# Kernel tuning notes

Hardware: AMD Instinct MI355X
Metric: run time of the kernel (lower is better)

The kernel has to match this reference:

```python
import jax, jax.numpy as jnp
from jax import lax
import numpy as np
import math

DIM = 96      # channels
HEADS = 3     # num_heads
WS = 8        # window size
SHIFT = 4     # window_size // 2 (depth is odd -> shifted)
TLC = 64      # tlc_kernel
H = 264
W = 264


def _grid_idxes(h, w, k1, k2):
    # Faithful replication of the torch grids() tiling index logic (static ints).
    num_row = (h - 1) // k1 + 1
    num_col = (w - 1) // k2 + 1
    step_j = k2 if num_col == 1 else math.ceil((w - k2) / (num_col - 1) - 1e-8)
    step_i = k1 if num_row == 1 else math.ceil((h - k1) / (num_row - 1) - 1e-8)
    idxes = []
    i = 0
    last_i = False
    while i < h and not last_i:
        j = 0
        if i + k1 >= h:
            i = h - k1
            last_i = True
        last_j = False
        while j < w and not last_j:
            if j + k2 >= w:
                j = w - k2
                last_j = True
            idxes.append((i, j))
            j = j + step_j
        i = i + step_i
    return idxes


def setup_inputs() -> dict:
    key = jax.random.key(0)
    ks = jax.random.split(key, 4)
    return {
        "x": jax.random.normal(ks[0], (1, DIM, H, W), jnp.float32),
        "temperature": jnp.ones((HEADS, 1, 1), jnp.float32),
        "qkv_w": jax.random.normal(ks[1], (3 * DIM, DIM), jnp.float32) * 0.05,
        "dw_w": jax.random.normal(ks[2], (3 * DIM, 1, 3, 3), jnp.float32) * 0.1,
        "proj_w": jax.random.normal(ks[3], (DIM, DIM), jnp.float32) * 0.05,
    }


def reference(x, temperature, qkv_w, dw_w, proj_w):
    b, c, h, w = x.shape
    # depth % 2 == 1 -> cyclic shift
    x = jnp.roll(x, (-SHIFT, -SHIFT), axis=(2, 3))
    # 1x1 pointwise conv (no bias)
    qkv = jnp.einsum('oc,bchw->bohw', qkv_w, x)
    # 3x3 depthwise conv, padding 1
    qkv = lax.conv_general_dilated(
        qkv, dw_w, window_strides=(1, 1), padding=[(1, 1), (1, 1)],
        feature_group_count=3 * c, dimension_numbers=('NCHW', 'OIHW', 'NCHW'))
    # --- TLC grids: overlapping tiles (eval path, b == 1) ---
    k1, k2 = min(h, TLC), min(w, TLC)
    idxes = _grid_idxes(h, w, k1, k2)
    parts = jnp.concatenate([qkv[:, :, i:i + k1, j:j + k2] for (i, j) in idxes], axis=0)  # [T,3c,k1,k2]
    T, C3, th, tw = parts.shape
    nh, nw = th // WS, tw // WS
    # window partition: b c (h b0) (w b1) -> (b h w) c b0 b1 -> flatten spatial
    win = parts.reshape(T, C3, nh, WS, nw, WS).transpose(0, 2, 4, 1, 3, 5)
    win = win.reshape(T * nh * nw, C3, WS * WS)  # [Bw, 3c, 64]
    q, k, v = jnp.split(win, 3, axis=1)  # each [Bw, c, 64]
    ch = c // HEADS
    q = q.reshape(-1, HEADS, ch, WS * WS)
    k = k.reshape(-1, HEADS, ch, WS * WS)
    v = v.reshape(-1, HEADS, ch, WS * WS)
    # L2 normalize along token dim (F.normalize eps=1e-12)
    q = q / jnp.maximum(jnp.linalg.norm(q, axis=-1, keepdims=True), 1e-12)
    k = k / jnp.maximum(jnp.linalg.norm(k, axis=-1, keepdims=True), 1e-12)
    # channel attention: [Bw, head, ch, ch]
    attn = jax.nn.relu(jnp.einsum('bhcn,bhdn->bhcd', q, k) * temperature)
    out = jnp.einsum('bhcd,bhdn->bhcn', attn, v)  # [Bw, head, ch, 64]
    out = out.reshape(-1, c, WS, WS)
    # window merge back to tiles
    out = out.reshape(T, nh, nw, c, WS, WS).transpose(0, 3, 1, 4, 2, 5).reshape(T, c, th, tw)
    # --- TLC grids_inverse: scatter-add overlapping tiles and average ---
    preds = jnp.zeros((b, c, h, w), x.dtype)
    cnt = np.zeros((h, w), np.float32)
    for t, (i, j) in enumerate(idxes):
        preds = preds.at[0, :, i:i + k1, j:j + k2].add(out[t])
        cnt[i:i + k1, j:j + k2] += 1.0
    preds = preds / jnp.asarray(cnt)
    # 1x1 output projection
    out = jnp.einsum('oc,bchw->bohw', proj_w, preds)
    # undo cyclic shift
    return jnp.roll(out, (SHIFT, SHIFT), axis=(2, 3))
```

## Files before the change

kernel.cpp:

```cpp
#include <hip/hip_runtime.h>
#include <hip/hip_bf16.h>

#define HW_ 69696
#define W_ 264
#define H_ 264

typedef short bf16x8 __attribute__((ext_vector_type(8)));
typedef float f32x4 __attribute__((ext_vector_type(4)));

static __device__ __forceinline__ unsigned short f2b(float f) {
  __hip_bfloat16 h = __float2bfloat16(f);
  return *reinterpret_cast<unsigned short*>(&h);
}
static __device__ __forceinline__ float b2f(unsigned short u) {
  __hip_bfloat16 h;
  *reinterpret_cast<unsigned short*>(&h) = u;
  return __bfloat162float(h);
}
static __device__ __forceinline__ float lo_f(unsigned int u) {
  union { unsigned int i; float f; } c; c.i = u << 16; return c.f;
}
static __device__ __forceinline__ float hi_f(unsigned int u) {
  union { unsigned int i; float f; } c; c.i = u & 0xffff0000u; return c.f;
}

__global__ __launch_bounds__(256, 3) void k_gemm(const float* __restrict__ x,
                                                 const float* __restrict__ w,
                                                 unsigned short* __restrict__ outb) {
  __shared__ __align__(16) char smem[46592];
  __shared__ int rp[128];
  unsigned short* As = (unsigned short*)smem;
  unsigned short* Bs = As + 96 * 104;

  const int tid = threadIdx.x;
  const int px0 = blockIdx.x * 128;
  const int oc = blockIdx.y;

  if (tid < 128) {
    int p = px0 + tid;
    int r = 0;
    if (p < HW_) {
      int y = p / W_, xx = p - y * W_;
      int y2 = y + 4; if (y2 >= H_) y2 -= H_;
      int x2 = xx + 4; if (x2 >= W_) x2 -= W_;
      r = y2 * W_ + x2;
    }
    rp[tid] = r;
  }

  const float* wp = w + oc * 96 * 96;
  for (int l = tid; l < 96 * 24; l += 256) {
    int o = l / 24, c4 = (l - (l / 24) * 24) * 4;
    float4 v = *(const float4*)&wp[o * 96 + c4];
    unsigned int p0 = (unsigned int)f2b(v.x) | ((unsigned int)f2b(v.y) << 16);
    unsigned int p1 = (unsigned int)f2b(v.z) | ((unsigned int)f2b(v.w) << 16);
    *(uint2*)&As[o * 104 + c4] = make_uint2(p0, p1);
  }
  __syncthreads();

  for (int l = tid; l < 128 * 12; l += 256) {
    int pxl = l & 127, g = l >> 7;
    uint4 o = make_uint4(0u, 0u, 0u, 0u);
    if (px0 + pxl < HW_) {
      const int base = rp[pxl];
      const float* xp = x + (size_t)(g * 8) * HW_ + base;
      float f0 = xp[0];
      float f1 = xp[HW_];
      float f2 = xp[2 * HW_];
      float f3 = xp[3 * HW_];
      float f4 = xp[4 * HW_];
      float f5 = xp[5 * HW_];
      float f6 = xp[6 * HW_];
      float f7 = xp[7 * HW_];
      o.x = (unsigned int)f2b(f0) | ((unsigned int)f2b(f1) << 16);
      o.y = (unsigned int)f2b(f2) | ((unsigned int)f2b(f3) << 16);
      o.z = (unsigned int)f2b(f4) | ((unsigned int)f2b(f5) << 16);
      o.w = (unsigned int)f2b(f6) | ((unsigned int)f2b(f7) << 16);
    }
    *(uint4*)&Bs[pxl * 104 + g * 8] = o;
  }
  __syncthreads();

  const int wid = tid >> 6, lane = tid & 63;
  const int quad = lane >> 4, lo = lane & 15;
  f32x4 acc[6][2];
#pragma unroll
  for (int mt = 0; mt < 6; ++mt)
#pragma unroll
    for (int nt = 0; nt < 2; ++nt) acc[mt][nt] = {0.f, 0.f, 0.f, 0.f};

#pragma unroll
  for (int ks = 0; ks < 3; ++ks) {
    const int kb = ks * 32 + quad * 8;
    bf16x8 b[2];
#pragma unroll
    for (int nt = 0; nt < 2; ++nt)
      b[nt] = *(const bf16x8*)&Bs[(wid * 32 + nt * 16 + lo) * 104 + kb];
#pragma unroll
    for (int mt = 0; mt < 6; ++mt) {
      bf16x8 a = *(const bf16x8*)&As[(mt * 16 + lo) * 104 + kb];
#pragma unroll
      for (int nt = 0; nt < 2; ++nt)
        acc[mt][nt] = __builtin_amdgcn_mfma_f32_16x16x32_bf16(a, b[nt], acc[mt][nt], 0, 0, 0);
    }
  }

  __syncthreads();
  unsigned short* Cs2 = (unsigned short*)smem;
#pragma unroll
  for (int mt = 0; mt < 6; ++mt)
#pragma unroll
    for (int nt = 0; nt < 2; ++nt) {
      int px_l = wid * 32 + nt * 16 + lo;
#pragma unroll
      for (int r = 0; r < 4; ++r)
        Cs2[px_l * 104 + mt * 16 + quad * 4 + r] = f2b(acc[mt][nt][r]);
    }
  __syncthreads();
  for (int i = tid; i < 128 * 12; i += 256) {
    int pxl = i & 127, j = i >> 7;
    if (px0 + pxl < HW_)
      *((uint4*)outb + (size_t)(oc * 12 + j) * HW_ + px0 + pxl) =
          ((const uint4*)(Cs2 + pxl * 104))[j];
  }
}

__global__ __launch_bounds__(256) void k_dw(const unsigned short* __restrict__ qkv,
                                            const float* __restrict__ dw,
                                            unsigned short* __restrict__ out) {
  __shared__ __align__(16) uint4 inS[18 * 66];
  const int tid = threadIdx.x;
  const int x0 = blockIdx.x * 64;
  const int y0 = blockIdx.y * 16;
  const int u = blockIdx.z;
  const uint4* plane = (const uint4*)qkv + (size_t)u * HW_;
  const float* wp = dw + u * 72;
  float wv[72];
#pragma unroll
  for (int i = 0; i < 72; ++i) wv[i] = wp[i];

  for (int idx = tid; idx < 18 * 66; idx += 256) {
    int rr = idx / 66, cc = idx - rr * 66;
    int gy = y0 - 1 + rr, gx = x0 - 1 + cc;
    uint4 v = make_uint4(0u, 0u, 0u, 0u);
    if ((unsigned)gy < (unsigned)H_ && (unsigned)gx < (unsigned)W_)
      v = plane[gy * W_ + gx];
    inS[idx] = v;
  }
  __syncthreads();

#pragma unroll
  for (int k = 0; k < 4; ++k) {
    const int oidx = k * 256 + tid;
    const int ro = oidx >> 6, co = oidx & 63;
    const int y = y0 + ro, x = x0 + co;
    float acc[8] = {0.f, 0.f, 0.f, 0.f, 0.f, 0.f, 0.f, 0.f};
#pragma unroll
    for (int dy = 0; dy < 3; ++dy)
#pragma unroll
      for (int dx = 0; dx < 3; ++dx) {
        uint4 v = inS[(ro + dy) * 66 + co + dx];
        float w0 = wv[0 * 9 + dy * 3 + dx], w1 = wv[1 * 9 + dy * 3 + dx];
        float w2 = wv[2 * 9 + dy * 3 + dx], w3 = wv[3 * 9 + dy * 3 + dx];
        float w4 = wv[4 * 9 + dy * 3 + dx], w5 = wv[5 * 9 + dy * 3 + dx];
        float w6 = wv[6 * 9 + dy * 3 + dx], w7 = wv[7 * 9 + dy * 3 + dx];
        acc[0] += w0 * lo_f(v.x); acc[1] += w1 * hi_f(v.x);
        acc[2] += w2 * lo_f(v.y); acc[3] += w3 * hi_f(v.y);
        acc[4] += w4 * lo_f(v.z); acc[5] += w5 * hi_f(v.z);
        acc[6] += w6 * lo_f(v.w); acc[7] += w7 * hi_f(v.w);
      }
    if (y < H_ && x < W_) {
      uint4 o;
      o.x = (unsigned int)f2b(acc[0]) | ((unsigned int)f2b(acc[1]) << 16);
      o.y = (unsigned int)f2b(acc[2]) | ((unsigned int)f2b(acc[3]) << 16);
      o.z = (unsigned int)f2b(acc[4]) | ((unsigned int)f2b(acc[5]) << 16);
      o.w = (unsigned int)f2b(acc[6]) | ((unsigned int)f2b(acc[7]) << 16);
      *((uint4*)out + (size_t)u * HW_ + y * W_ + x) = o;
    }
  }
}

#define P1 200
#define P8 1608
__global__ __launch_bounds__(192) void k_attn(const unsigned short* __restrict__ qd,
                                              const float* __restrict__ temp,
                                              unsigned short* __restrict__ tout) {
  __shared__ __align__(16) unsigned short flat[8 * P8];
  __shared__ __align__(16) unsigned short attnL[3 * 32 * 40];
  __shared__ float invn[3 * 32];
  const int tid = threadIdx.x;
  const int wi = blockIdx.x, t = blockIdx.y;
  const int i0 = (t / 5) * 50, j0 = (t % 5) * 50;
  const int wy = wi >> 3, wx = wi & 7;
  const int gy0 = i0 + wy * 8, gx0 = j0 + wx * 8;

  {
    const size_t base = (size_t)gy0 * W_ + gx0;
    for (int idx = tid; idx < 24 * 64; idx += 192) {
      int u = idx >> 6, rj = idx & 63, r = rj >> 3, j = rj & 7;
      uint4 v = ((const uint4*)qd)[(size_t)u * HW_ + base + r * W_ + j];
      ((uint4*)flat)[r * 201 + j * 25 + u] = v;
    }
  }
  __syncthreads();

  const int h = tid >> 6, lane = tid & 63;
  const int quad = lane >> 4, lo = lane & 15;
  const int cb = h * 32;

  bf16x8 qf[2][2], kf[2][2];
#pragma unroll
  for (int mt = 0; mt < 2; ++mt)
#pragma unroll
    for (int kt = 0; kt < 2; ++kt) {
      const int rbase = (kt * 4 + quad) * P8;
      const int cq = cb + mt * 16 + lo;
      const int ck = 96 + cb + mt * 16 + lo;
      bf16x8 q8, k8;
#pragma unroll
      for (int j = 0; j < 8; ++j) {
        q8[j] = (short)flat[rbase + j * P1 + cq];
        k8[j] = (short)flat[rbase + j * P1 + ck];
      }
      qf[mt][kt] = q8;
      kf[mt][kt] = k8;
    }

  f32x4 S[2][2];
#pragma unroll
  for (int mt = 0; mt < 2; ++mt)
#pragma unroll
    for (int nt = 0; nt < 2; ++nt) {
      S[mt][nt] = {0.f, 0.f, 0.f, 0.f};
#pragma unroll
      for (int kt = 0; kt < 2; ++kt)
        S[mt][nt] = __builtin_amdgcn_mfma_f32_16x16x32_bf16(qf[mt][kt], kf[nt][kt], S[mt][nt], 0, 0, 0);
    }

  float ivk[2];
#pragma unroll
  for (int mt = 0; mt < 2; ++mt) {
    float sq = 0.f, sk = 0.f;
#pragma unroll
    for (int kt = 0; kt < 2; ++kt)
#pragma unroll
      for (int j = 0; j < 8; ++j) {
        float a = b2f((unsigned short)qf[mt][kt][j]);
        float b = b2f((unsigned short)kf[mt][kt][j]);
        sq += a * a;
        sk += b * b;
      }
    sq += __shfl_xor(sq, 16);
    sq += __shfl_xor(sq, 32);
    sk += __shfl_xor(sk, 16);
    sk += __shfl_xor(sk, 32);
    if (quad == 0) invn[h * 32 + mt * 16 + lo] = 1.f / fmaxf(sqrtf(sq), 1e-12f);
    ivk[mt] = 1.f / fmaxf(sqrtf(sk), 1e-12f);
  }
  __syncthreads();

  const float ts = temp[h];
#pragma unroll
  for (int mt = 0; mt < 2; ++mt)
#pragma unroll
    for (int nt = 0; nt < 2; ++nt)
#pragma unroll
      for (int r = 0; r < 4; ++r) {
        int c = mt * 16 + quad * 4 + r;
        float v = S[mt][nt][r] * invn[h * 32 + c] * ivk[nt] * ts;
        attnL[(h * 32 + c) * 40 + nt * 16 + lo] = f2b(fmaxf(v, 0.f));
      }
  __syncthreads();

  bf16x8 af[2];
#pragma unroll
  for (int mt = 0; mt < 2; ++mt)
    af[mt] = *(const bf16x8*)&attnL[(h * 32 + mt * 16 + lo) * 40 + quad * 8];

  const int uv = 24 + h * 4 + quad;
  f32x4 O[2][4];
#pragma unroll
  for (int nt = 0; nt < 4; ++nt) {
    const int px = nt * 16 + lo;
    const size_t gpx = (size_t)(gy0 + (px >> 3)) * W_ + gx0 + (px & 7);
    uint4 vraw = ((const uint4*)qd)[(size_t)uv * HW_ + gpx];
    bf16x8 vf = *reinterpret_cast<bf16x8*>(&vraw);
#pragma unroll
    for (int mt = 0; mt < 2; ++mt) {
      f32x4 z = {0.f, 0.f, 0.f, 0.f};
      O[mt][nt] = __builtin_amdgcn_mfma_f32_16x16x32_bf16(af[mt], vf, z, 0, 0, 0);
    }
  }
  __syncthreads();

  unsigned short* Cs = flat;
#pragma unroll
  for (int mt = 0; mt < 2; ++mt)
#pragma unroll
    for (int nt = 0; nt < 4; ++nt) {
      const int px = nt * 16 + lo;
      unsigned int p0 = (unsigned int)f2b(O[mt][nt][0]) | ((unsigned int)f2b(O[mt][nt][1]) << 16);
      unsigned int p1 = (unsigned int)f2b(O[mt][nt][2]) | ((unsigned int)f2b(O[mt][nt][3]) << 16);
      *(uint2*)&Cs[px * 104 + cb + mt * 16 + quad * 4] = make_uint2(p0, p1);
    }
  __syncthreads();

  for (int idx = tid; idx < 64 * 12; idx += 192) {
    int rec = idx / 12, u = idx - (idx / 12) * 12;
    int r = rec >> 3, j = rec & 7;
    size_t g = (size_t)t * 4096 + (wy * 8 + r) * 64 + wx * 8 + j;
    ((uint4*)tout)[g * 12 + u] = ((const uint4*)(Cs + rec * 104))[u];
  }
}

__global__ __launch_bounds__(256, 4) void k_avgproj(const float* __restrict__ w,
                                                    const unsigned short* __restrict__ tout,
                                                    float* __restrict__ outf) {
  __shared__ __align__(16) char smem[33280];
  unsigned short* As = (unsigned short*)smem;
  unsigned short* Bs = As + 96 * 104;

  const int tid = threadIdx.x;
  const int px0 = blockIdx.x * 64;

  for (int l = tid; l < 96 * 24; l += 256) {
    int o = l / 24, c4 = (l - (l / 24) * 24) * 4;
    float4 v = *(const float4*)&w[o * 96 + c4];
    unsigned int p0 = (unsigned int)f2b(v.x) | ((unsigned int)f2b(v.y) << 16);
    unsigned int p1 = (unsigned int)f2b(v.z) | ((unsigned int)f2b(v.w) << 16);
    *(uint2*)&As[o * 104 + c4] = make_uint2(p0, p1);
  }

  {
    const int pxl = tid >> 2, q = tid & 3;
    const int px = px0 + pxl;
    unsigned short* bd = Bs + pxl * 104 + q * 24;
    const int y = px / W_, xx = px - y * W_;
    int loy = (y >= 64) ? (y - 14) / 50 : 0;
    int hiy = y / 50; if (hiy > 4) hiy = 4;
    int lox = (xx >= 64) ? (xx - 14) / 50 : 0;
    int hix = xx / 50; if (hix > 4) hix = 4;
    float acc[24];
#pragma unroll
    for (int i = 0; i < 24; ++i) acc[i] = 0.f;
    int cnt = 0;
    for (int ty = loy; ty <= hiy; ++ty)
      for (int tx = lox; tx <= hix; ++tx) {
        size_t rec = (size_t)(ty * 5 + tx) * 4096 + ((y - ty * 50) << 6) + (xx - tx * 50);
        const uint4* rp = (const uint4*)tout + rec * 12 + q * 3;
#pragma unroll
        for (int ui = 0; ui < 3; ++ui) {
          uint4 v = rp[ui];
          acc[ui * 8 + 0] += lo_f(v.x); acc[ui * 8 + 1] += hi_f(v.x);
          acc[ui * 8 + 2] += lo_f(v.y); acc[ui * 8 + 3] += hi_f(v.y);
          acc[ui * 8 + 4] += lo_f(v.z); acc[ui * 8 + 5] += hi_f(v.z);
          acc[ui * 8 + 6] += lo_f(v.w); acc[ui * 8 + 7] += hi_f(v.w);
        }
        ++cnt;
      }
    const float inv = 1.f / (float)cnt;
#pragma unroll
    for (int ui = 0; ui < 3; ++ui) {
      uint4 o;
      o.x = (unsigned int)f2b(acc[ui * 8 + 0] * inv) | ((unsigned int)f2b(acc[ui * 8 + 1] * inv) << 16);
      o.y = (unsigned int)f2b(acc[ui * 8 + 2] * inv) | ((unsigned int)f2b(acc[ui * 8 + 3] * inv) << 16);
      o.z = (unsigned int)f2b(acc[ui * 8 + 4] * inv) | ((unsigned int)f2b(acc[ui * 8 + 5] * inv) << 16);
      o.w = (unsigned int)f2b(acc[ui * 8 + 6] * inv) | ((unsigned int)f2b(acc[ui * 8 + 7] * inv) << 16);
      ((uint4*)bd)[ui] = o;
    }
  }
  __syncthreads();

  const int wid = tid >> 6, lane = tid & 63;
  const int quad = lane >> 4, lo = lane & 15;
  f32x4 acc[6];
#pragma unroll
  for (int mt = 0; mt < 6; ++mt) acc[mt] = {0.f, 0.f, 0.f, 0.f};

#pragma unroll
  for (int ks = 0; ks < 3; ++ks) {
    const int kb = ks * 32 + quad * 8;
    bf16x8 b = *(const bf16x8*)&Bs[(wid * 16 + lo) * 104 + kb];
#pragma unroll
    for (int mt = 0; mt < 6; ++mt) {
      bf16x8 a = *(const bf16x8*)&As[(mt * 16 + lo) * 104 + kb];
      acc[mt] = __builtin_amdgcn_mfma_f32_16x16x32_bf16(a, b, acc[mt], 0, 0, 0);
    }
  }

  {
    int px = px0 + wid * 16 + lo;
    int y = px / W_, xx = px - y * W_;
    int y2 = y + 4; if (y2 >= H_) y2 -= H_;
    int x2 = xx + 4; if (x2 >= W_) x2 -= W_;
    int tp = y2 * W_ + x2;
#pragma unroll
    for (int mt = 0; mt < 6; ++mt) {
      int row = mt * 16 + quad * 4;
#pragma unroll
      for (int r = 0; r < 4; ++r)
        outf[(size_t)(row + r) * HW_ + tp] = acc[mt][r];
    }
  }
}

extern "C" void kernel_launch(void* const* d_in, const int* in_sizes, int n_in,
                              void* d_out, int out_size, void* d_ws, size_t ws_size,
                              hipStream_t stream) {
  (void)in_sizes; (void)n_in; (void)out_size; (void)ws_size;
  const float* x = (const float*)d_in[0];
  const float* temp = (const float*)d_in[1];
  const float* qkvw = (const float*)d_in[2];
  const float* dww = (const float*)d_in[3];
  const float* projw = (const float*)d_in[4];
  float* out = (float*)d_out;

  char* ws = (char*)d_ws;
  const size_t SZQ = (size_t)288 * HW_ * 2;
  unsigned short* qkvb = (unsigned short*)ws;
  unsigned short* tout = (unsigned short*)ws;
  unsigned short* qkvd = (unsigned short*)(ws + SZQ);

  k_gemm<<<dim3(545, 3), 256, 0, stream>>>(x, qkvw, qkvb);
  k_dw<<<dim3(5, 17, 36), 256, 0, stream>>>(qkvb, dww, qkvd);
  k_attn<<<dim3(64, 25), 192, 0, stream>>>(qkvd, temp, tout);
  k_avgproj<<<dim3(1089), 256, 0, stream>>>(projw, tout, out);
}
```

Before: 163.4 us.

## Fuse depthwise conv into window attention kernel, computing halo per window

Merges the separate depthwise 3x3 conv kernel into the attention kernel: each attention block loads a 10x10 halo of the pointwise qkv output for its 8x8 window, convolves in registers, and writes q/k/v directly into shared memory. This removes the write and re-read of the full depthwise output tensor and one kernel launch. The cost is redundant halo loads and repeated convolution for overlapping tiles (25 tiles of 64x64 overlap), plus much larger shared memory use per block, which may lower occupancy.

```diff
diff --git a/kernel.cpp b/kernel.cpp
--- a/kernel.cpp
+++ b/kernel.cpp
@@ -125,84 +125,73 @@
   }
 }
 
-__global__ __launch_bounds__(256) void k_dw(const unsigned short* __restrict__ qkv,
-                                            const float* __restrict__ dw,
-                                            unsigned short* __restrict__ out) {
-  __shared__ __align__(16) uint4 inS[18 * 66];
+#define FP1 200
+__global__ __launch_bounds__(192) void k_dwattn(const unsigned short* __restrict__ qkv,
+                                                const float* __restrict__ dw,
+                                                const float* __restrict__ temp,
+                                                unsigned short* __restrict__ tout) {
+  __shared__ __align__(16) char smem[59456];
+  uint4* sIn = (uint4*)smem;
+  unsigned short* flat = (unsigned short*)(smem + 20160);
+  unsigned short* vS = (unsigned short*)(smem + 45760);
+  float* invn = (float*)(smem + 59072);
+  unsigned short* attnL = (unsigned short*)smem;
+  unsigned short* Cs = flat;
+
   const int tid = threadIdx.x;
-  const int x0 = blockIdx.x * 64;
-  const int y0 = blockIdx.y * 16;
-  const int u = blockIdx.z;
-  const uint4* plane = (const uint4*)qkv + (size_t)u * HW_;
-  const float* wp = dw + u * 72;
-  float wv[72];
-#pragma unroll
-  for (int i = 0; i < 72; ++i) wv[i] = wp[i];
-
-  for (int idx = tid; idx < 18 * 66; idx += 256) {
-    int rr = idx / 66, cc = idx - rr * 66;
-    int gy = y0 - 1 + rr, gx = x0 - 1 + cc;
-    uint4 v = make_uint4(0u, 0u, 0u, 0u);
-    if ((unsigned)gy < (unsigned)H_ && (unsigned)gx < (unsigned)W_)
-      v = plane[gy * W_ + gx];
-    inS[idx] = v;
-  }
-  __syncthreads();
-
-#pragma unroll
-  for (int k = 0; k < 4; ++k) {
-    const int oidx = k * 256 + tid;
-    const int ro = oidx >> 6, co = oidx & 63;
-    const int y = y0 + ro, x = x0 + co;
-    float acc[8] = {0.f, 0.f, 0.f, 0.f, 0.f, 0.f, 0.f, 0.f};
-#pragma unroll
-    for (int dy = 0; dy < 3; ++dy)
-#pragma unroll
-      for (int dx = 0; dx < 3; ++dx) {
-        uint4 v = inS[(ro + dy) * 66 + co + dx];
-        float w0 = wv[0 * 9 + dy * 3 + dx], w1 = wv[1 * 9 + dy * 3 + dx];
-        float w2 = wv[2 * 9 + dy * 3 + dx], w3 = wv[3 * 9 + dy * 3 + dx];
-        float w4 = wv[4 * 9 + dy * 3 + dx], w5 = wv[5 * 9 + dy * 3 + dx];
-        float w6 = wv[6 * 9 + dy * 3 + dx], w7 = wv[7 * 9 + dy * 3 + dx];
-        acc[0] += w0 * lo_f(v.x); acc[1] += w1 * hi_f(v.x);
-        acc[2] += w2 * lo_f(v.y); acc[3] += w3 * hi_f(v.y);
-        acc[4] += w4 * lo_f(v.z); acc[5] += w5 * hi_f(v.z);
-        acc[6] += w6 * lo_f(v.w); acc[7] += w7 * hi_f(v.w);
-      }
-    if (y < H_ && x < W_) {
+  const int wi = blockIdx.x, t = blockIdx.y;
+  const int i0 = (t / 5) * 50, j0 = (t % 5) * 50;
+  const int wy = wi >> 3, wx = wi & 7;
+  const int gy0 = i0 + wy * 8, gx0 = j0 + wx * 8;
+
+  const int cuu = tid >> 4;
+  const int cs = tid & 15;
+
+#pragma unroll
+  for (int c3 = 0; c3 < 3; ++c3) {
+    for (int idx = tid; idx < 1200; idx += 192) {
+      int uu = idx / 100, p = idx - uu * 100;
+      int r = p / 10, j = p - r * 10;
+      int gy = gy0 - 1 + r, gx = gx0 - 1 + j;
+      uint4 v = make_uint4(0u, 0u, 0u, 0u);
+      if ((unsigned)gy < (unsigned)H_ && (unsigned)gx < (unsigned)W_)
+        v = ((const uint4*)qkv)[(size_t)(c3 * 12 + uu) * HW_ + gy * W_ + gx];
+      sIn[uu * 105 + p] = v;
+    }
+    float wv[72];
+    {
+      const float* wp = dw + (c3 * 12 + cuu) * 72;
+#pragma unroll
+      for (int i = 0; i < 72; ++i) wv[i] = wp[i];
+    }
+    __syncthreads();
+#pragma unroll
+    for (int k = 0; k < 4; ++k) {
+      const int px = cs + k * 16;
+      const int r = px >> 3, j = px & 7;
+      float acc[8] = {0.f, 0.f, 0.f, 0.f, 0.f, 0.f, 0.f, 0.f};
+#pragma unroll
+      for (int dy = 0; dy < 3; ++dy)
+#pragma unroll
+        for (int dx = 0; dx < 3; ++dx) {
+          uint4 v = sIn[cuu * 105 + (r + dy) * 10 + (j + dx)];
+          const int tp = dy * 3 + dx;
+          acc[0] += wv[0 * 9 + tp] * lo_f(v.x); acc[1] += wv[1 * 9 + tp] * hi_f(v.x);
+          acc[2] += wv[2 * 9 + tp] * lo_f(v.y); acc[3] += wv[3 * 9 + tp] * hi_f(v.y);
+          acc[4] += wv[4 * 9 + tp] * lo_f(v.z); acc[5] += wv[5 * 9 + tp] * hi_f(v.z);
+          acc[6] += wv[6 * 9 + tp] * lo_f(v.w); acc[7] += wv[7 * 9 + tp] * hi_f(v.w);
+        }
       uint4 o;
       o.x = (unsigned int)f2b(acc[0]) | ((unsigned int)f2b(acc[1]) << 16);
       o.y = (unsigned int)f2b(acc[2]) | ((unsigned int)f2b(acc[3]) << 16);
       o.z = (unsigned int)f2b(acc[4]) | ((unsigned int)f2b(acc[5]) << 16);
       o.w = (unsigned int)f2b(acc[6]) | ((unsigned int)f2b(acc[7]) << 16);
-      *((uint4*)out + (size_t)u * HW_ + y * W_ + x) = o;
-    }
-  }
-}
-
-#define P1 200
-#define P8 1608
-__global__ __launch_bounds__(192) void k_attn(const unsigned short* __restrict__ qd,
-                                              const float* __restrict__ temp,
-                                              unsigned short* __restrict__ tout) {
-  __shared__ __align__(16) unsigned short flat[8 * P8];
-  __shared__ __align__(16) unsigned short attnL[3 * 32 * 40];
-  __shared__ float invn[3 * 32];
-  const int tid = threadIdx.x;
-  const int wi = blockIdx.x, t = blockIdx.y;
-  const int i0 = (t / 5) * 50, j0 = (t % 5) * 50;
-  const int wy = wi >> 3, wx = wi & 7;
-  const int gy0 = i0 + wy * 8, gx0 = j0 + wx * 8;
-
-  {
-    const size_t base = (size_t)gy0 * W_ + gx0;
-    for (int idx = tid; idx < 24 * 64; idx += 192) {
-      int u = idx >> 6, rj = idx & 63, r = rj >> 3, j = rj & 7;
-      uint4 v = ((const uint4*)qd)[(size_t)u * HW_ + base + r * W_ + j];
-      ((uint4*)flat)[r * 201 + j * 25 + u] = v;
-    }
-  }
-  __syncthreads();
+      if (c3 == 0) *(uint4*)&flat[px * FP1 + cuu * 8] = o;
+      else if (c3 == 1) *(uint4*)&flat[px * FP1 + 96 + cuu * 8] = o;
+      else *(uint4*)&vS[px * 104 + cuu * 8] = o;
+    }
+    __syncthreads();
+  }
 
   const int h = tid >> 6, lane = tid & 63;
   const int quad = lane >> 4, lo = lane & 15;
@@ -213,14 +202,14 @@
   for (int mt = 0; mt < 2; ++mt)
 #pragma unroll
     for (int kt = 0; kt < 2; ++kt) {
-      const int rbase = (kt * 4 + quad) * P8;
+      const int rbase = ((kt * 4 + quad) * 8) * FP1;
       const int cq = cb + mt * 16 + lo;
       const int ck = 96 + cb + mt * 16 + lo;
       bf16x8 q8, k8;
 #pragma unroll
       for (int j = 0; j < 8; ++j) {
-        q8[j] = (short)flat[rbase + j * P1 + cq];
-        k8[j] = (short)flat[rbase + j * P1 + ck];
+        q8[j] = (short)flat[rbase + j * FP1 + cq];
+        k8[j] = (short)flat[rbase + j * FP1 + ck];
       }
       qf[mt][kt] = q8;
       kf[mt][kt] = k8;
@@ -277,14 +266,11 @@
   for (int mt = 0; mt < 2; ++mt)
     af[mt] = *(const bf16x8*)&attnL[(h * 32 + mt * 16 + lo) * 40 + quad * 8];
 
-  const int uv = 24 + h * 4 + quad;
   f32x4 O[2][4];
 #pragma unroll
   for (int nt = 0; nt < 4; ++nt) {
     const int px = nt * 16 + lo;
-    const size_t gpx = (size_t)(gy0 + (px >> 3)) * W_ + gx0 + (px & 7);
-    uint4 vraw = ((const uint4*)qd)[(size_t)uv * HW_ + gpx];
-    bf16x8 vf = *reinterpret_cast<bf16x8*>(&vraw);
+    bf16x8 vf = *(const bf16x8*)&vS[px * 104 + cb + quad * 8];
 #pragma unroll
     for (int mt = 0; mt < 2; ++mt) {
       f32x4 z = {0.f, 0.f, 0.f, 0.f};
@@ -293,7 +279,6 @@
   }
   __syncthreads();
 
-  unsigned short* Cs = flat;
 #pragma unroll
   for (int mt = 0; mt < 2; ++mt)
 #pragma unroll
@@ -418,11 +403,9 @@
   char* ws = (char*)d_ws;
   const size_t SZQ = (size_t)288 * HW_ * 2;
   unsigned short* qkvb = (unsigned short*)ws;
-  unsigned short* tout = (unsigned short*)ws;
-  unsigned short* qkvd = (unsigned short*)(ws + SZQ);
+  unsigned short* tout = (unsigned short*)(ws + SZQ);
 
   k_gemm<<<dim3(545, 3), 256, 0, stream>>>(x, qkvw, qkvb);
-  k_dw<<<dim3(5, 17, 36), 256, 0, stream>>>(qkvb, dww, qkvd);
-  k_attn<<<dim3(64, 25), 192, 0, stream>>>(qkvd, temp, tout);
+  k_dwattn<<<dim3(64, 25), 192, 0, stream>>>(qkvb, dww, temp, tout);
   k_avgproj<<<dim3(1089), 256, 0, stream>>>(projw, tout, out);
 }
```

Measured after the change: 190.4 us. 16.5% more time.

## Load GEMM B operands directly into MFMA registers and loop output chunks per block

Applied to the files above, without the earlier changes.

The QKV GEMM now has each lane read its own shifted input pixels straight into bf16 MFMA B fragments in registers. It drops the LDS staging of the input tile, and each block loops over all three output-channel chunks, so the x tile is read from global memory once rather than three times. The avg-proj kernel likewise builds its B fragment in registers from the tile averaging instead of going through shared memory. Together these cut LDS usage, barriers and redundant global reads, at the cost of more sequential work per block and uncoalesced strided per-lane loads.

```diff
diff --git a/kernel.cpp b/kernel.cpp
--- a/kernel.cpp
+++ b/kernel.cpp
@@ -24,104 +24,77 @@
   union { unsigned int i; float f; } c; c.i = u & 0xffff0000u; return c.f;
 }
 
-__global__ __launch_bounds__(256, 3) void k_gemm(const float* __restrict__ x,
+__global__ __launch_bounds__(256, 4) void k_gemm(const float* __restrict__ x,
                                                  const float* __restrict__ w,
                                                  unsigned short* __restrict__ outb) {
-  __shared__ __align__(16) char smem[46592];
-  __shared__ int rp[128];
+  __shared__ __align__(16) char smem[19968];
   unsigned short* As = (unsigned short*)smem;
-  unsigned short* Bs = As + 96 * 104;
+  unsigned short* Cs = (unsigned short*)smem;
 
   const int tid = threadIdx.x;
-  const int px0 = blockIdx.x * 128;
-  const int oc = blockIdx.y;
-
-  if (tid < 128) {
-    int p = px0 + tid;
-    int r = 0;
-    if (p < HW_) {
-      int y = p / W_, xx = p - y * W_;
-      int y2 = y + 4; if (y2 >= H_) y2 -= H_;
-      int x2 = xx + 4; if (x2 >= W_) x2 -= W_;
-      r = y2 * W_ + x2;
-    }
-    rp[tid] = r;
-  }
-
-  const float* wp = w + oc * 96 * 96;
-  for (int l = tid; l < 96 * 24; l += 256) {
-    int o = l / 24, c4 = (l - (l / 24) * 24) * 4;
-    float4 v = *(const float4*)&wp[o * 96 + c4];
-    unsigned int p0 = (unsigned int)f2b(v.x) | ((unsigned int)f2b(v.y) << 16);
-    unsigned int p1 = (unsigned int)f2b(v.z) | ((unsigned int)f2b(v.w) << 16);
-    *(uint2*)&As[o * 104 + c4] = make_uint2(p0, p1);
-  }
-  __syncthreads();
-
-  for (int l = tid; l < 128 * 12; l += 256) {
-    int pxl = l & 127, g = l >> 7;
-    uint4 o = make_uint4(0u, 0u, 0u, 0u);
-    if (px0 + pxl < HW_) {
-      const int base = rp[pxl];
-      const float* xp = x + (size_t)(g * 8) * HW_ + base;
-      float f0 = xp[0];
-      float f1 = xp[HW_];
-      float f2 = xp[2 * HW_];
-      float f3 = xp[3 * HW_];
-      float f4 = xp[4 * HW_];
-      float f5 = xp[5 * HW_];
-      float f6 = xp[6 * HW_];
-      float f7 = xp[7 * HW_];
-      o.x = (unsigned int)f2b(f0) | ((unsigned int)f2b(f1) << 16);
-      o.y = (unsigned int)f2b(f2) | ((unsigned int)f2b(f3) << 16);
-      o.z = (unsigned int)f2b(f4) | ((unsigned int)f2b(f5) << 16);
-      o.w = (unsigned int)f2b(f6) | ((unsigned int)f2b(f7) << 16);
-    }
-    *(uint4*)&Bs[pxl * 104 + g * 8] = o;
-  }
-  __syncthreads();
-
   const int wid = tid >> 6, lane = tid & 63;
   const int quad = lane >> 4, lo = lane & 15;
-  f32x4 acc[6][2];
-#pragma unroll
-  for (int mt = 0; mt < 6; ++mt)
-#pragma unroll
-    for (int nt = 0; nt < 2; ++nt) acc[mt][nt] = {0.f, 0.f, 0.f, 0.f};
-
+  const int px0 = blockIdx.x * 64;
+  const int px = px0 + wid * 16 + lo;
+
+  const int y = px / W_, xx = px - y * W_;
+  int y2 = y + 4; if (y2 >= H_) y2 -= H_;
+  int x2 = xx + 4; if (x2 >= W_) x2 -= W_;
+  const float* xb = x + y2 * W_ + x2;
+
+  bf16x8 bf[3];
 #pragma unroll
   for (int ks = 0; ks < 3; ++ks) {
-    const int kb = ks * 32 + quad * 8;
-    bf16x8 b[2];
-#pragma unroll
-    for (int nt = 0; nt < 2; ++nt)
-      b[nt] = *(const bf16x8*)&Bs[(wid * 32 + nt * 16 + lo) * 104 + kb];
+    const float* xp = xb + (size_t)(ks * 32 + quad * 8) * HW_;
+    float f[8];
+#pragma unroll
+    for (int i = 0; i < 8; ++i) f[i] = xp[(size_t)i * HW_];
+    union { bf16x8 v; unsigned short s[8]; } u;
+#pragma unroll
+    for (int i = 0; i < 8; ++i) u.s[i] = f2b(f[i]);
+    bf[ks] = u.v;
+  }
+
+  for (int oc = 0; oc < 3; ++oc) {
+    __syncthreads();
+    const float* wp = w + oc * 96 * 96;
+    for (int l = tid; l < 96 * 24; l += 256) {
+      int o = l / 24, c4 = (l - (l / 24) * 24) * 4;
+      float4 v = *(const float4*)&wp[o * 96 + c4];
+      unsigned int p0 = (unsigned int)f2b(v.x) | ((unsigned int)f2b(v.y) << 16);
+      unsigned int p1 = (unsigned int)f2b(v.z) | ((unsigned int)f2b(v.w) << 16);
+      *(uint2*)&As[o * 104 + c4] = make_uint2(p0, p1);
+    }
+    __syncthreads();
+
+    f32x4 acc[6];
+#pragma unroll
+    for (int mt = 0; mt < 6; ++mt) acc[mt] = {0.f, 0.f, 0.f, 0.f};
+#pragma unroll
+    for (int ks = 0; ks < 3; ++ks) {
+      const int kb = ks * 32 + quad * 8;
+#pragma unroll
+      for (int mt = 0; mt < 6; ++mt) {
+        bf16x8 a = *(const bf16x8*)&As[(mt * 16 + lo) * 104 + kb];
+        acc[mt] = __builtin_amdgcn_mfma_f32_16x16x32_bf16(a, bf[ks], acc[mt], 0, 0, 0);
+      }
+    }
+    __syncthreads();
+
+    const int pxl = wid * 16 + lo;
 #pragma unroll
     for (int mt = 0; mt < 6; ++mt) {
-      bf16x8 a = *(const bf16x8*)&As[(mt * 16 + lo) * 104 + kb];
-#pragma unroll
-      for (int nt = 0; nt < 2; ++nt)
-        acc[mt][nt] = __builtin_amdgcn_mfma_f32_16x16x32_bf16(a, b[nt], acc[mt][nt], 0, 0, 0);
-    }
-  }
-
-  __syncthreads();
-  unsigned short* Cs2 = (unsigned short*)smem;
-#pragma unroll
-  for (int mt = 0; mt < 6; ++mt)
-#pragma unroll
-    for (int nt = 0; nt < 2; ++nt) {
-      int px_l = wid * 32 + nt * 16 + lo;
-#pragma unroll
-      for (int r = 0; r < 4; ++r)
-        Cs2[px_l * 104 + mt * 16 + quad * 4 + r] = f2b(acc[mt][nt][r]);
-    }
-  __syncthreads();
-  for (int i = tid; i < 128 * 12; i += 256) {
-    int pxl = i & 127, j = i >> 7;
-    if (px0 + pxl < HW_)
-      *((uint4*)outb + (size_t)(oc * 12 + j) * HW_ + px0 + pxl) =
-          ((const uint4*)(Cs2 + pxl * 104))[j];
+      unsigned int p0 = (unsigned int)f2b(acc[mt][0]) | ((unsigned int)f2b(acc[mt][1]) << 16);
+      unsigned int p1 = (unsigned int)f2b(acc[mt][2]) | ((unsigned int)f2b(acc[mt][3]) << 16);
+      *(uint2*)&Cs[pxl * 104 + mt * 16 + quad * 4] = make_uint2(p0, p1);
+    }
+    __syncthreads();
+
+    for (int i = tid; i < 64 * 12; i += 256) {
+      int pxl2 = i & 63, j = i >> 6;
+      *((uint4*)outb + (size_t)(oc * 12 + j) * HW_ + px0 + pxl2) =
+          ((const uint4*)(Cs + pxl2 * 104))[j];
+    }
   }
 }
 
@@ -316,12 +289,12 @@
 __global__ __launch_bounds__(256, 4) void k_avgproj(const float* __restrict__ w,
                                                     const unsigned short* __restrict__ tout,
                                                     float* __restrict__ outf) {
-  __shared__ __align__(16) char smem[33280];
-  unsigned short* As = (unsigned short*)smem;
-  unsigned short* Bs = As + 96 * 104;
-
+  __shared__ __align__(16) unsigned short As[96 * 104];
   const int tid = threadIdx.x;
+  const int wid = tid >> 6, lane = tid & 63;
+  const int quad = lane >> 4, lo = lane & 15;
   const int px0 = blockIdx.x * 64;
+  const int px = px0 + wid * 16 + lo;
 
   for (int l = tid; l < 96 * 24; l += 256) {
     int o = l / 24, c4 = (l - (l / 24) * 24) * 4;
@@ -331,66 +304,54 @@
     *(uint2*)&As[o * 104 + c4] = make_uint2(p0, p1);
   }
 
-  {
-    const int pxl = tid >> 2, q = tid & 3;
-    const int px = px0 + pxl;
-    unsigned short* bd = Bs + pxl * 104 + q * 24;
-    const int y = px / W_, xx = px - y * W_;
-    int loy = (y >= 64) ? (y - 14) / 50 : 0;
-    int hiy = y / 50; if (hiy > 4) hiy = 4;
-    int lox = (xx >= 64) ? (xx - 14) / 50 : 0;
-    int hix = xx / 50; if (hix > 4) hix = 4;
-    float acc[24];
-#pragma unroll
-    for (int i = 0; i < 24; ++i) acc[i] = 0.f;
-    int cnt = 0;
-    for (int ty = loy; ty <= hiy; ++ty)
-      for (int tx = lox; tx <= hix; ++tx) {
-        size_t rec = (size_t)(ty * 5 + tx) * 4096 + ((y - ty * 50) << 6) + (xx - tx * 50);
-        const uint4* rp = (const uint4*)tout + rec * 12 + q * 3;
-#pragma unroll
-        for (int ui = 0; ui < 3; ++ui) {
-          uint4 v = rp[ui];
-          acc[ui * 8 + 0] += lo_f(v.x); acc[ui * 8 + 1] += hi_f(v.x);
-          acc[ui * 8 + 2] += lo_f(v.y); acc[ui * 8 + 3] += hi_f(v.y);
-          acc[ui * 8 + 4] += lo_f(v.z); acc[ui * 8 + 5] += hi_f(v.z);
-          acc[ui * 8 + 6] += lo_f(v.w); acc[ui * 8 + 7] += hi_f(v.w);
-        }
-        ++cnt;
-      }
-    const float inv = 1.f / (float)cnt;
-#pragma unroll
-    for (int ui = 0; ui < 3; ++ui) {
-      uint4 o;
-      o.x = (unsigned int)f2b(acc[ui * 8 + 0] * inv) | ((unsigned int)f2b(acc[ui * 8 + 1] * inv) << 16);
-      o.y = (unsigned int)f2b(acc[ui * 8 + 2] * inv) | ((unsigned int)f2b(acc[ui * 8 + 3] * inv) << 16);
-      o.z = (unsigned int)f2b(acc[ui * 8 + 4] * inv) | ((unsigned int)f2b(acc[ui * 8 + 5] * inv) << 16);
-      o.w = (unsigned int)f2b(acc[ui * 8 + 6] * inv) | ((unsigned int)f2b(acc[ui * 8 + 7] * inv) << 16);
-      ((uint4*)bd)[ui] = o;
-    }
-  }
-  __syncthreads();
-
-  const int wid = tid >> 6, lane = tid & 63;
-  const int quad = lane >> 4, lo = lane & 15;
+  const int y = px / W_, xx = px - y * W_;
+  int loy = (y >= 64) ? (y - 14) / 50 : 0;
+  int hiy = y / 50; if (hiy > 4) hiy = 4;
+  int lox = (xx >= 64) ? (xx - 14) / 50 : 0;
+  int hix = xx / 50; if (hix > 4) hix = 4;
+  float a24[24];
+#pragma unroll
+  for (int i = 0; i < 24; ++i) a24[i] = 0.f;
+  int cnt = 0;
+  for (int ty = loy; ty <= hiy; ++ty)
+    for (int tx = lox; tx <= hix; ++tx) {
+      size_t rec = (size_t)(ty * 5 + tx) * 4096 + ((y - ty * 50) << 6) + (xx - tx * 50);
+      const uint4* rp = (const uint4*)tout + rec * 12 + quad;
+#pragma unroll
+      for (int ks = 0; ks < 3; ++ks) {
+        uint4 v = rp[ks * 4];
+        a24[ks * 8 + 0] += lo_f(v.x); a24[ks * 8 + 1] += hi_f(v.x);
+        a24[ks * 8 + 2] += lo_f(v.y); a24[ks * 8 + 3] += hi_f(v.y);
+        a24[ks * 8 + 4] += lo_f(v.z); a24[ks * 8 + 5] += hi_f(v.z);
+        a24[ks * 8 + 6] += lo_f(v.w); a24[ks * 8 + 7] += hi_f(v.w);
+      }
+      ++cnt;
+    }
+  const float inv = 1.f / (float)cnt;
+  bf16x8 bf[3];
+#pragma unroll
+  for (int ks = 0; ks < 3; ++ks) {
+    union { bf16x8 v; unsigned short s[8]; } u;
+#pragma unroll
+    for (int i = 0; i < 8; ++i) u.s[i] = f2b(a24[ks * 8 + i] * inv);
+    bf[ks] = u.v;
+  }
+  __syncthreads();
+
   f32x4 acc[6];
 #pragma unroll
   for (int mt = 0; mt < 6; ++mt) acc[mt] = {0.f, 0.f, 0.f, 0.f};
-
 #pragma unroll
   for (int ks = 0; ks < 3; ++ks) {
     const int kb = ks * 32 + quad * 8;
-    bf16x8 b = *(const bf16x8*)&Bs[(wid * 16 + lo) * 104 + kb];
 #pragma unroll
     for (int mt = 0; mt < 6; ++mt) {
       bf16x8 a = *(const bf16x8*)&As[(mt * 16 + lo) * 104 + kb];
-      acc[mt] = __builtin_amdgcn_mfma_f32_16x16x32_bf16(a, b, acc[mt], 0, 0, 0);
+      acc[mt] = __builtin_amdgcn_mfma_f32_16x16x32_bf16(a, bf[ks], acc[mt], 0, 0, 0);
     }
   }
 
   {
-    int px = px0 + wid * 16 + lo;
-    int y = px / W_, xx = px - y * W_;
     int y2 = y + 4; if (y2 >= H_) y2 -= H_;
     int x2 = xx + 4; if (x2 >= W_) x2 -= W_;
     int tp = y2 * W_ + x2;
@@ -421,7 +382,7 @@
   unsigned short* tout = (unsigned short*)ws;
   unsigned short* qkvd = (unsigned short*)(ws + SZQ);
 
-  k_gemm<<<dim3(545, 3), 256, 0, stream>>>(x, qkvw, qkvb);
+  k_gemm<<<dim3(1089), 256, 0, stream>>>(x, qkvw, qkvb);
   k_dw<<<dim3(5, 17, 36), 256, 0, stream>>>(qkvb, dww, qkvd);
   k_attn<<<dim3(64, 25), 192, 0, stream>>>(qkvd, temp, tout);
   k_avgproj<<<dim3(1089), 256, 0, stream>>>(projw, tout, out);
```

New measurement: 150.1 us, median of 2. -8.1%, faster.
